# Kernel tuning notes

Hardware: AMD Instinct MI355X
Metric: run time of the kernel (lower is better)

## Reference

```python
import jax, jax.numpy as jnp
import numpy as np

B, T, C = 1, 2048, 2048
N_HEADS, N_KV_HEADS = 32, 8
D_HEAD = C // N_HEADS  # 64
WINDOW = 512
ROPE_BASE = 10000.0


def setup_inputs() -> dict:
    key = jax.random.key(0)
    ks = jax.random.split(key, 5)
    s = 0.02
    return {
        "x": jax.random.normal(ks[0], (B, T, C), dtype=jnp.float32),
        "wq": jax.random.normal(ks[1], (C, N_HEADS * D_HEAD), dtype=jnp.float32) * s,
        "wk": jax.random.normal(ks[2], (C, N_KV_HEADS * D_HEAD), dtype=jnp.float32) * s,
        "wv": jax.random.normal(ks[3], (C, N_KV_HEADS * D_HEAD), dtype=jnp.float32) * s,
        "wo": jax.random.normal(ks[4], (N_HEADS * D_HEAD, C), dtype=jnp.float32) * s,
    }


def _rope_tables(seq_len, d_head, dtype):
    inv_freq = 1.0 / (ROPE_BASE ** (jnp.arange(0, d_head, 2, dtype=jnp.float32) / d_head))
    t = jnp.arange(seq_len, dtype=jnp.float32)
    freqs = t[:, None] * inv_freq[None, :]          # [T, d/2]
    emb = jnp.concatenate([freqs, freqs], axis=-1)  # [T, d]
    return jnp.cos(emb).astype(dtype), jnp.sin(emb).astype(dtype)


def _rotate_half(u):
    d = u.shape[-1]
    return jnp.concatenate([-u[..., d // 2:], u[..., :d // 2]], axis=-1)


def reference(x, wq, wk, wv, wo):
    b, t, c = x.shape
    n_rep = N_HEADS // N_KV_HEADS
    q = (x @ wq).reshape(b, t, N_HEADS, D_HEAD)
    k = (x @ wk).reshape(b, t, N_KV_HEADS, D_HEAD)
    v = (x @ wv).reshape(b, t, N_KV_HEADS, D_HEAD)

    cos, sin = _rope_tables(t, D_HEAD, x.dtype)
    cos = cos[None, :, None, :]
    sin = sin[None, :, None, :]
    q = q * cos + _rotate_half(q) * sin
    k = k * cos + _rotate_half(k) * sin

    # repeat_interleave KV heads up to n_heads (GQA expansion)
    k = jnp.repeat(k, n_rep, axis=2)  # [B,T,H,d]
    v = jnp.repeat(v, n_rep, axis=2)

    scale = 1.0 / np.sqrt(D_HEAD)
    scores = jnp.einsum('bqhd,bkhd->bhqk', q, k) * scale  # [B,H,T,T]

    # sliding-window causal mask: attend iff k<=q and q-k<=window
    qi = jnp.arange(t)[:, None]
    ki = jnp.arange(t)[None, :]
    allowed = (ki <= qi) & (qi - ki <= WINDOW)  # [T,T] bool
    scores = jnp.where(allowed[None, None, :, :], scores, -jnp.inf)

    attn = jax.nn.softmax(scores, axis=-1)
    out = jnp.einsum('bhqk,bkhd->bqhd', attn, v).reshape(b, t, N_HEADS * D_HEAD)
    return out @ wo
```

## Files before the change

### kernel.cpp

```cpp
#include <hip/hip_runtime.h>
#include <hip/hip_bf16.h>
#include <math.h>

#define T_SEQ 2048
#define C_DIM 2048
#define NH    32
#define NKV   8
#define DH    64
#define WIN   512
#define QKV_N 3072

typedef __bf16 bf16x8 __attribute__((ext_vector_type(8)));
typedef __bf16 bf16x4 __attribute__((ext_vector_type(4)));
typedef float  f32x4  __attribute__((ext_vector_type(4)));

#if __has_builtin(__builtin_amdgcn_exp2f)
#define EXP2(x) __builtin_amdgcn_exp2f(x)
#else
#define EXP2(x) exp2f(x)
#endif

__device__ __forceinline__ void gload_lds16(const __bf16* g, __bf16* l) {
  __builtin_amdgcn_global_load_lds(
      (const __attribute__((address_space(1))) void*)g,
      (__attribute__((address_space(3))) void*)l, 16, 0, 0);
}

__device__ __forceinline__ void tr_tile(const float* __restrict__ in,
                                        __bf16* __restrict__ out,
                                        int R, int Ccols, int tile, int tid,
                                        float (*sh)[33]) {
  int tpc = Ccols >> 5;
  int c0 = (tile % tpc) << 5;
  int r0 = (tile / tpc) << 5;
  int tx = tid & 31, ty = tid >> 5;
#pragma unroll
  for (int i = 0; i < 32; i += 8)
    sh[ty + i][tx] = in[(size_t)(r0 + ty + i) * Ccols + c0 + tx];
  __syncthreads();
#pragma unroll
  for (int i = 0; i < 32; i += 8)
    out[(size_t)(c0 + ty + i) * R + r0 + tx] = (__bf16)sh[tx][ty + i];
}

__global__ __launch_bounds__(256) void prep_kernel(
    const float* __restrict__ x, const float* __restrict__ wq,
    const float* __restrict__ wk, const float* __restrict__ wv,
    __bf16* __restrict__ xb, __bf16* __restrict__ wqkvT,
    float2* __restrict__ tab) {
  __shared__ float sh[32][33];
  int bid = blockIdx.x;
  const int tid = threadIdx.x;
  if (bid < 4096) {
    int i = bid * 256 + tid;
    float4 v = ((const float4*)x)[i];
    bf16x4 o = {(__bf16)v.x, (__bf16)v.y, (__bf16)v.z, (__bf16)v.w};
    *(bf16x4*)(xb + (size_t)i * 4) = o;
    return;
  }
  bid -= 4096;
  if (bid < 256) {
    int i = bid * 256 + tid;
    int j = i & 31, t = i >> 5;
    float inv = powf(10000.0f, -(float)(2 * j) / 64.0f);
    float s, c;
    sincosf((float)t * inv, &s, &c);
    tab[i] = make_float2(c, s);
    return;
  }
  bid -= 256;
  if (bid < 4096) { tr_tile(wq, wqkvT, C_DIM, C_DIM, bid, tid, sh); return; }
  bid -= 4096;
  if (bid < 1024) {
    tr_tile(wk, wqkvT + (size_t)2048 * C_DIM, C_DIM, NKV * DH, bid, tid, sh);
    return;
  }
  bid -= 1024;
  tr_tile(wv, wqkvT + (size_t)2560 * C_DIM, C_DIM, NKV * DH, bid, tid, sh);
}

template <typename OutT, bool ROPE>
__global__ __launch_bounds__(512) void gemm_bf16_kernel(
    const __bf16* __restrict__ A, const __bf16* __restrict__ Bt,
    OutT* __restrict__ C, const float2* __restrict__ rope_tab,
    int M, int N, int K, int chx, int chy) {
  __shared__ __bf16 As[2][128 * 64];
  __shared__ __bf16 Bs[2][64 * 64];

  const int tid = threadIdx.x;
  const int wid = tid >> 6, l = tid & 63;
  const int lm = l & 15, lh = l >> 4;

  const int hw  = blockIdx.x;
  const int xcd = hw & 7;
  const int idx = hw >> 3;
  const int bx  = (xcd & 3) * chx + idx % chx;
  const int by  = (xcd >> 2) * chy + idx / chx;
  const int brow = by * 128, bcol = bx * 64;

  const int kb_swz = (((l & 7) ^ (l >> 3)) << 3);
  const int srow   = l >> 3;

  auto stage = [&](int kbase, int bi) {
#pragma unroll
    for (int c = 0; c < 3; ++c) {
      int ci = wid + c * 8;
      if (ci < 16) {
        int row = ci * 8 + srow;
        gload_lds16(A + (size_t)(brow + row) * K + kbase + kb_swz,
                    &As[bi][ci * 512]);
      } else {
        int row = (ci - 16) * 8 + srow;
        gload_lds16(Bt + (size_t)(bcol + row) * K + kbase + kb_swz,
                    &Bs[bi][(ci - 16) * 512]);
      }
    }
  };

  f32x4 acc[4] = {};
  const int NT = K >> 6;

  stage(0, 0);
  __syncthreads();

  for (int t = 0; t < NT; ++t) {
    const int cur = t & 1;
    if (t + 1 < NT) stage((t + 1) << 6, cur ^ 1);

    const __bf16* as = As[cur];
    const __bf16* bs = Bs[cur];
    const int x7 = lm & 7;
    bf16x8 af[2], bfr[4][2];
#pragma unroll
    for (int u = 0; u < 2; ++u)
      af[u] = *(const bf16x8*)&as[(wid * 16 + lm) * 64 +
                                  (((u * 4 + lh) ^ x7) << 3)];
#pragma unroll
    for (int j = 0; j < 4; ++j)
#pragma unroll
      for (int u = 0; u < 2; ++u)
        bfr[j][u] = *(const bf16x8*)&bs[(j * 16 + lm) * 64 +
                                        (((u * 4 + lh) ^ x7) << 3)];
#pragma unroll
    for (int u = 0; u < 2; ++u)
#pragma unroll
      for (int j = 0; j < 4; ++j)
        acc[j] = __builtin_amdgcn_mfma_f32_16x16x32_bf16(
            af[u], bfr[j][u], acc[j], 0, 0, 0);

    __syncthreads();
  }

  if (ROPE) {
    if (bcol < 2560) {
#pragma unroll
      for (int r = 0; r < 4; ++r) {
        int t = brow + wid * 16 + lh * 4 + r;
#pragma unroll
        for (int j = 0; j < 2; ++j) {
          float2 cs = rope_tab[t * 32 + j * 16 + lm];
          float v0 = acc[j][r], v1 = acc[j + 2][r];
          acc[j][r]     = v0 * cs.x - v1 * cs.y;
          acc[j + 2][r] = v1 * cs.x + v0 * cs.y;
        }
      }
    }
    if (bcol < 2048) {
#pragma unroll
      for (int j = 0; j < 4; ++j)
#pragma unroll
        for (int r = 0; r < 4; ++r) acc[j][r] *= 0.18033688f;
    }
  }

#pragma unroll
  for (int j = 0; j < 4; ++j)
#pragma unroll
    for (int r = 0; r < 4; ++r) {
      int row = brow + wid * 16 + lh * 4 + r;
      int col = bcol + j * 16 + lm;
      C[(size_t)row * N + col] = (OutT)acc[j][r];
    }
}

__global__ __launch_bounds__(256) void attn_mfma_kernel(
    const __bf16* __restrict__ QKV, __bf16* __restrict__ O,
    const float* __restrict__ wo, __bf16* __restrict__ woT) {
  const int tid = threadIdx.x;

  if (blockIdx.x >= 1024) {
    __shared__ float sh[32][33];
    tr_tile(wo, woT, C_DIM, C_DIM, blockIdx.x - 1024, tid, sh);
    return;
  }

  __shared__ __bf16 K_lds[64][72];
  __shared__ __bf16 Vt[64][72];
  __shared__ __bf16 P_lds[4][16][72];

  const int bid = (((int)blockIdx.x & 7) << 7) + ((int)blockIdx.x >> 3);

  const int l   = tid & 63;
  const int w   = tid >> 6;
  const int q0  = (bid & 31) * 64;
  const int h   = bid >> 5;
  const int kvh = h >> 2;
  const int q0w = q0 + w * 16;
  const int lm  = l & 15;
  const int lh  = l >> 4;

  const __bf16* Qp = QKV + h * DH;
  const __bf16* Kp = QKV + 2048 + kvh * DH;
  const __bf16* Vp = QKV + 2560 + kvh * DH;

  bf16x8 aq0 = *(const bf16x8*)(Qp + (size_t)(q0w + lm) * QKV_N + lh * 8);
  bf16x8 aq1 = *(const bf16x8*)(Qp + (size_t)(q0w + lm) * QKV_N + 32 + lh * 8);

  f32x4 o_acc[4] = {};
  float m = -60.0f, lsum = 0.0f;

  const int klo  = (q0 - WIN) > 0 ? (q0 - WIN) : 0;
  const int skey = tid >> 2;
  const int sdp  = (tid & 3) * 16;

  for (int k0 = klo; k0 < q0 + 64; k0 += 64) {
    __syncthreads();
    {
      const __bf16* ks = Kp + (size_t)(k0 + skey) * QKV_N + sdp;
      *(bf16x8*)&K_lds[skey][sdp]     = *(const bf16x8*)ks;
      *(bf16x8*)&K_lds[skey][sdp + 8] = *(const bf16x8*)(ks + 8);
      const __bf16* vs = Vp + (size_t)(k0 + l) * QKV_N + w * 16;
      bf16x8 v0 = *(const bf16x8*)vs;
      bf16x8 v1 = *(const bf16x8*)(vs + 8);
#pragma unroll
      for (int j = 0; j < 8; ++j) Vt[w * 16 + j][l]     = v0[j];
#pragma unroll
      for (int j = 0; j < 8; ++j) Vt[w * 16 + 8 + j][l] = v1[j];
    }
    __syncthreads();

    f32x4 s[4] = {};
#pragma unroll
    for (int kg = 0; kg < 4; ++kg) {
      bf16x8 kb0 = *(const bf16x8*)&K_lds[kg * 16 + lm][lh * 8];
      bf16x8 kb1 = *(const bf16x8*)&K_lds[kg * 16 + lm][32 + lh * 8];
      s[kg] = __builtin_amdgcn_mfma_f32_16x16x32_bf16(kb0, aq0, s[kg], 0, 0, 0);
      s[kg] = __builtin_amdgcn_mfma_f32_16x16x32_bf16(kb1, aq1, s[kg], 0, 0, 0);
    }

    float sv[4][4];
    const bool full = (k0 + 63 <= q0w) && (k0 >= q0w + 15 - WIN);
    if (full) {
#pragma unroll
      for (int kg = 0; kg < 4; ++kg)
#pragma unroll
        for (int r = 0; r < 4; ++r) sv[kg][r] = s[kg][r];
    } else {
      const int qr = q0w + lm;
#pragma unroll
      for (int kg = 0; kg < 4; ++kg)
#pragma unroll
        for (int r = 0; r < 4; ++r) {
          int kc = k0 + kg * 16 + lh * 4 + r;
          sv[kg][r] = (kc <= qr && kc + WIN >= qr) ? s[kg][r] : -1e30f;
        }
    }

    float t01 = fmaxf(fmaxf(fmaxf(sv[0][0], sv[0][1]), fmaxf(sv[0][2], sv[0][3])),
                      fmaxf(fmaxf(sv[1][0], sv[1][1]), fmaxf(sv[1][2], sv[1][3])));
    float t23 = fmaxf(fmaxf(fmaxf(sv[2][0], sv[2][1]), fmaxf(sv[2][2], sv[2][3])),
                      fmaxf(fmaxf(sv[3][0], sv[3][1]), fmaxf(sv[3][2], sv[3][3])));
    float tmax = fmaxf(t01, t23);
    tmax = fmaxf(tmax, __shfl_xor(tmax, 16));
    tmax = fmaxf(tmax, __shfl_xor(tmax, 32));

    if (!__all(tmax <= m + 8.0f)) {
      float mn = fmaxf(m, tmax);
      float co = EXP2(m - mn);
      m = mn;
      lsum *= co;
#pragma unroll
      for (int dc = 0; dc < 4; ++dc)
#pragma unroll
        for (int r = 0; r < 4; ++r) o_acc[dc][r] *= co;
    }
    float ps = 0.0f;
#pragma unroll
    for (int kg = 0; kg < 4; ++kg)
#pragma unroll
      for (int r = 0; r < 4; ++r) {
        float p = EXP2(sv[kg][r] - m);
        sv[kg][r] = p;
        ps += p;
      }
    ps += __shfl_xor(ps, 16);
    ps += __shfl_xor(ps, 32);
    lsum += ps;

#pragma unroll
    for (int kg = 0; kg < 4; ++kg) {
      bf16x4 pw;
#pragma unroll
      for (int r = 0; r < 4; ++r) pw[r] = (__bf16)sv[kg][r];
      *(bf16x4*)&P_lds[w][lm][kg * 16 + lh * 4] = pw;
    }
    bf16x8 pf0 = *(const bf16x8*)&P_lds[w][lm][lh * 8];
    bf16x8 pf1 = *(const bf16x8*)&P_lds[w][lm][32 + lh * 8];

#pragma unroll
    for (int dc = 0; dc < 4; ++dc) {
      bf16x8 vb0 = *(const bf16x8*)&Vt[dc * 16 + lm][lh * 8];
      bf16x8 vb1 = *(const bf16x8*)&Vt[dc * 16 + lm][32 + lh * 8];
      o_acc[dc] = __builtin_amdgcn_mfma_f32_16x16x32_bf16(vb0, pf0, o_acc[dc], 0, 0, 0);
      o_acc[dc] = __builtin_amdgcn_mfma_f32_16x16x32_bf16(vb1, pf1, o_acc[dc], 0, 0, 0);
    }
  }

  const float inv = 1.0f / lsum;
#pragma unroll
  for (int dc = 0; dc < 4; ++dc) {
    bf16x4 ov;
#pragma unroll
    for (int r = 0; r < 4; ++r) ov[r] = (__bf16)(o_acc[dc][r] * inv);
    *(bf16x4*)&O[(size_t)(q0w + lm) * C_DIM + h * DH + dc * 16 + lh * 4] = ov;
  }
}

extern "C" void kernel_launch(void* const* d_in, const int* in_sizes, int n_in,
                              void* d_out, int out_size, void* d_ws, size_t ws_size,
                              hipStream_t stream) {
  const float* x  = (const float*)d_in[0];
  const float* wq = (const float*)d_in[1];
  const float* wk = (const float*)d_in[2];
  const float* wv = (const float*)d_in[3];
  const float* wo = (const float*)d_in[4];
  float* out = (float*)d_out;

  __bf16* xb    = (__bf16*)d_ws;
  __bf16* wqkvT = xb + (size_t)C_DIM * C_DIM;
  __bf16* woT   = wqkvT + (size_t)QKV_N * C_DIM;
  __bf16* QKV   = woT + (size_t)C_DIM * C_DIM;
  float2* tab   = (float2*)(QKV + (size_t)T_SEQ * QKV_N);
  __bf16* Ab    = xb;

  prep_kernel<<<4096 + 256 + 4096 + 1024 + 1024, 256, 0, stream>>>(
      x, wq, wk, wv, xb, wqkvT, tab);

  gemm_bf16_kernel<__bf16, true>
      <<<768, 512, 0, stream>>>(
          xb, wqkvT, QKV, tab, T_SEQ, QKV_N, C_DIM, 12, 8);

  attn_mfma_kernel<<<1024 + 4096, 256, 0, stream>>>(QKV, Ab, wo, woT);

  gemm_bf16_kernel<float, false>
      <<<512, 512, 0, stream>>>(
          Ab, woT, out, nullptr, T_SEQ, C_DIM, C_DIM, 8, 8);
}
```

Before: 107.7 us.

## Use a 128x128-tile double-buffered GEMM for the output projection

New measurement: 111.4 us. 1.03x slower.

```diff
diff --git a/kernel.cpp b/kernel.cpp
--- a/kernel.cpp
+++ b/kernel.cpp
@@ -183,6 +183,94 @@
     }
 }
 
+template <typename OutT>
+__global__ __launch_bounds__(512) void gemm128_bf16_kernel(
+    const __bf16* __restrict__ A, const __bf16* __restrict__ Bt,
+    OutT* __restrict__ C, int M, int N, int K, int chx, int chy) {
+  __shared__ __bf16 As[2][128 * 64];
+  __shared__ __bf16 Bs[2][128 * 64];
+
+  const int tid = threadIdx.x;
+  const int wid = tid >> 6, l = tid & 63;
+  const int wr = wid >> 1, wc = wid & 1;
+  const int lm = l & 15, lh = l >> 4;
+
+  const int hw  = blockIdx.x;
+  const int xcd = hw & 7;
+  const int idx = hw >> 3;
+  const int bx  = (xcd & 3) * chx + idx % chx;
+  const int by  = (xcd >> 2) * chy + idx / chx;
+  const int brow = by * 128, bcol = bx * 128;
+
+  const int kb_swz = (((l & 7) ^ (l >> 3)) << 3);
+  const int srow   = l >> 3;
+
+  auto stage = [&](int kbase, int bi) {
+#pragma unroll
+    for (int c = 0; c < 4; ++c) {
+      int ci = wid + c * 8;
+      if (ci < 16) {
+        int row = ci * 8 + srow;
+        gload_lds16(A + (size_t)(brow + row) * K + kbase + kb_swz,
+                    &As[bi][ci * 512]);
+      } else {
+        int row = (ci - 16) * 8 + srow;
+        gload_lds16(Bt + (size_t)(bcol + row) * K + kbase + kb_swz,
+                    &Bs[bi][(ci - 16) * 512]);
+      }
+    }
+  };
+
+  f32x4 acc[2][4] = {};
+  const int NT = K >> 6;
+
+  stage(0, 0);
+  __syncthreads();
+
+  for (int t = 0; t < NT; ++t) {
+    const int cur = t & 1;
+    if (t + 1 < NT) stage((t + 1) << 6, cur ^ 1);
+
+    const __bf16* as = As[cur];
+    const __bf16* bs = Bs[cur];
+    const int x7 = lm & 7;
+    bf16x8 af[2][2], bfr[4][2];
+#pragma unroll
+    for (int i = 0; i < 2; ++i)
+#pragma unroll
+      for (int u = 0; u < 2; ++u)
+        af[i][u] = *(const bf16x8*)&as[(wr * 32 + i * 16 + lm) * 64 +
+                                       (((u * 4 + lh) ^ x7) << 3)];
+#pragma unroll
+    for (int j = 0; j < 4; ++j)
+#pragma unroll
+      for (int u = 0; u < 2; ++u)
+        bfr[j][u] = *(const bf16x8*)&bs[(wc * 64 + j * 16 + lm) * 64 +
+                                        (((u * 4 + lh) ^ x7) << 3)];
+#pragma unroll
+    for (int u = 0; u < 2; ++u)
+#pragma unroll
+      for (int i = 0; i < 2; ++i)
+#pragma unroll
+        for (int j = 0; j < 4; ++j)
+          acc[i][j] = __builtin_amdgcn_mfma_f32_16x16x32_bf16(
+              af[i][u], bfr[j][u], acc[i][j], 0, 0, 0);
+
+    __syncthreads();
+  }
+
+#pragma unroll
+  for (int i = 0; i < 2; ++i)
+#pragma unroll
+    for (int j = 0; j < 4; ++j)
+#pragma unroll
+      for (int r = 0; r < 4; ++r) {
+        int row = brow + wr * 32 + i * 16 + lh * 4 + r;
+        int col = bcol + wc * 64 + j * 16 + lm;
+        C[(size_t)row * N + col] = (OutT)acc[i][j][r];
+      }
+}
+
 __global__ __launch_bounds__(256) void attn_mfma_kernel(
     const __bf16* __restrict__ QKV, __bf16* __restrict__ O,
     const float* __restrict__ wo, __bf16* __restrict__ woT) {
@@ -352,7 +440,7 @@
 
   attn_mfma_kernel<<<1024 + 4096, 256, 0, stream>>>(QKV, Ab, wo, woT);
 
-  gemm_bf16_kernel<float, false>
-      <<<512, 512, 0, stream>>>(
-          Ab, woT, out, nullptr, T_SEQ, C_DIM, C_DIM, 8, 8);
-}
+  gemm128_bf16_kernel<float>
+      <<<256, 512, 0, stream>>>(
+          Ab, woT, out, T_SEQ, C_DIM, C_DIM, 4, 8);
+}
```
